# Kernel tuning notes

Hardware: AMD Instinct MI355X
Metric: run time of the kernel (lower is better)

Reference implementation:

```python
import jax, jax.numpy as jnp
import numpy as np

N_MEL, N_HID, N_ATT, N_TXT = 80, 1024, 640, 640

def lstm_cell(x, h, c, Wih, Whh, b):
    # torch LSTM gate order: i, f, g, o; b = b_ih + b_hh
    z = x @ Wih.T + h @ Whh.T + b
    i, f, g, o = jnp.split(z, 4, axis=-1)
    c = jax.nn.sigmoid(f) * c + jax.nn.sigmoid(i) * jnp.tanh(g)
    h = jax.nn.sigmoid(o) * jnp.tanh(c)
    return h, c

def setup_inputs() -> dict:
    key = jax.random.key(0)
    ks = jax.random.split(key, 32)
    s = 0.02
    p = {}
    p['residual'] = jax.random.normal(ks[0], (600, 1, N_MEL), jnp.float32)
    p['text'] = jax.random.normal(ks[1], (200, 1, N_TXT), jnp.float32)
    # attention LSTM (input n_mel -> hidden n_hid)
    p['Wih_a'] = jax.random.normal(ks[2], (4 * N_HID, N_MEL)) * s
    p['Whh_a'] = jax.random.normal(ks[3], (4 * N_HID, N_HID)) * s
    p['b_a'] = jax.random.normal(ks[4], (4 * N_HID,)) * s
    # attention projections (no bias)
    p['Wq'] = jax.random.normal(ks[5], (N_ATT, N_HID)) * s
    p['Wk'] = jax.random.normal(ks[6], (N_ATT, N_TXT)) * s
    p['Wv'] = jax.random.normal(ks[7], (N_ATT, N_TXT)) * s
    p['v_attn'] = jax.random.normal(ks[8], (N_ATT,)) * s
    # main 2-layer LSTM (input n_hid+n_att -> n_hid)
    p['Wih0'] = jax.random.normal(ks[9], (4 * N_HID, N_HID + N_ATT)) * s
    p['Whh0'] = jax.random.normal(ks[10], (4 * N_HID, N_HID)) * s
    p['b0'] = jax.random.normal(ks[11], (4 * N_HID,)) * s
    p['Wih1'] = jax.random.normal(ks[12], (4 * N_HID, N_HID)) * s
    p['Whh1'] = jax.random.normal(ks[13], (4 * N_HID, N_HID)) * s
    p['b1'] = jax.random.normal(ks[14], (4 * N_HID,)) * s
    # dense layer: two tanh linears
    p['Wd1'] = jax.random.normal(ks[15], (N_HID, N_HID)) * s
    p['bd1'] = jax.random.normal(ks[16], (N_HID,)) * s
    p['Wd2'] = jax.random.normal(ks[17], (N_HID, N_HID)) * s
    p['bd2'] = jax.random.normal(ks[18], (N_HID,)) * s
    # 1x1 conv == linear n_hid -> 2*n_mel
    p['Wc'] = jax.random.normal(ks[19], (2 * N_MEL, N_HID)) * s
    p['bc'] = jax.random.normal(ks[20], (2 * N_MEL,)) * s
    # gate layer
    p['Wg'] = jax.random.normal(ks[21], (1, N_HID + N_ATT)) * s
    p['bg'] = jax.random.normal(ks[22], (1,)) * s
    return p

def reference(residual, text, Wih_a, Whh_a, b_a, Wq, Wk, Wv, v_attn,
              Wih0, Whh0, b0, Wih1, Whh1, b1, Wd1, bd1, Wd2, bd2,
              Wc, bc, Wg, bg):
    T, B, n_mel = residual.shape
    H = Whh_a.shape[1]
    keys = text @ Wk.T          # (Tt, B, A)  precomputed, constant over steps
    vals = text @ Wv.T          # (Tt, B, A)
    res_flip = residual[::-1]   # AR_Back_Step flips time before the AR pass

    def step(carry, r_t):
        last_out, ha, ca, h0, c0, h1, c1 = carry
        ha, ca = lstm_cell(last_out, ha, ca, Wih_a, Whh_a, b_a)
        q = ha @ Wq.T                                   # (B, A)
        scores = jnp.tanh(q[None] + keys) @ v_attn      # (Tt, B)
        attn = jax.nn.softmax(scores, axis=0)
        ctx = jnp.einsum('tb,tba->ba', attn, vals)      # (B, A)
        dec_in = jnp.concatenate([ha, ctx], axis=-1)    # (B, H+A)
        h0, c0 = lstm_cell(dec_in, h0, c0, Wih0, Whh0, b0)
        h1, c1 = lstm_cell(h0, h1, c1, Wih1, Whh1, b1)
        d = jnp.tanh(jnp.tanh(h1 @ Wd1.T + bd1) @ Wd2.T + bd2)
        dec_out = d @ Wc.T + bc                         # (B, 2*n_mel)
        log_s, bb = dec_out[:, :n_mel], dec_out[:, n_mel:]
        out = (r_t - bb) * jnp.exp(-log_s)              # inverse affine coupling
        gate = jax.nn.sigmoid(dec_in @ Wg.T + bg)       # (B, 1)
        return (out, ha, ca, h0, c0, h1, c1), (out, gate)

    z = jnp.zeros((B, H), residual.dtype)
    init = (jnp.zeros((B, n_mel), residual.dtype), z, z, z, z, z, z)
    _, (outs, gates) = jax.lax.scan(step, init, res_flip)
    return outs[::-1], gates
```

## Files before the change

### kernel.cpp

```cpp
#include <hip/hip_runtime.h>
#include <hip/hip_bf16.h>
#include <math.h>

#define GBK 256
#define NT  512

constexpr int T_STEPS = 600;
constexpr int TXT     = 200;
constexpr int NMEL    = 80;
constexpr int H       = 1024;
constexpr int ATT     = 640;
constexpr int DIN     = H + ATT;
constexpr int GATE_B  = 200;
constexpr int NPH     = 8;
constexpr int NREP    = 8;

constexpr size_t O_WQ    = 0;
constexpr size_t O_WIHA  = O_WQ   + (size_t)ATT*H;
constexpr size_t O_WIH0  = O_WIHA + (size_t)4*H*NMEL;
constexpr size_t O_WHH1  = O_WIH0 + (size_t)4*H*DIN;
constexpr size_t O_WD1   = O_WHH1 + (size_t)4*H*H;
constexpr size_t O_WD2   = O_WD1  + (size_t)H*H;
constexpr size_t O_KEYS  = O_WD2  + (size_t)H*H;
constexpr size_t O_VALS  = O_KEYS + (size_t)TXT*ATT;
constexpr size_t O_END_U = O_VALS + (size_t)TXT*ATT;
constexpr size_t RBYTE   = ((O_END_U*2 + 255)/256)*256;
constexpr int RECN = NREP*NPH*GBK*8;

typedef unsigned short ushortT;
typedef ushortT us4 __attribute__((ext_vector_type(4)));
typedef ushortT us8 __attribute__((ext_vector_type(8)));
typedef unsigned uv2 __attribute__((ext_vector_type(2)));
typedef unsigned uv4 __attribute__((ext_vector_type(4)));

__device__ __forceinline__ float bf2f(ushortT u) {
  return __uint_as_float(((unsigned)u) << 16);
}
__device__ __forceinline__ ushortT f2bf(float x) {
  __hip_bfloat16 h = __float2bfloat16(x);
  ushortT u; __builtin_memcpy(&u, &h, 2); return u;
}
__device__ __forceinline__ us4 cvt4(float4 a) {
  return us4{ f2bf(a.x), f2bf(a.y), f2bf(a.z), f2bf(a.w) };
}
__device__ __forceinline__ float sigf(float x) { return 1.0f / (1.0f + expf(-x)); }
__device__ __forceinline__ float tanhfast(float x) {
  float e = __expf(2.0f * x);
  return (e - 1.0f) / (e + 1.0f);
}

__device__ __forceinline__ float red64(float v) {
  #pragma unroll
  for (int off = 32; off > 0; off >>= 1) v += __shfl_xor(v, off, 64);
  return v;
}

__device__ __forceinline__ unsigned* recptr(unsigned* R, int rep, int p, int b) {
  return R + ((size_t)((rep*NPH + p)*GBK + b) * 8);
}

__device__ __forceinline__ void rpub_pair(unsigned* R, int p, int b, int pairIdx,
                                          float v, unsigned e) {
  uv2 d; d.x = __float_as_uint(v); d.y = e;
  #pragma unroll
  for (int rep = 0; rep < NREP; ++rep) {
    unsigned* ptr = recptr(R, rep, p, b) + pairIdx*2;
    asm volatile("global_store_dwordx2 %0, %1, off sc0 sc1"
                 :: "v"(ptr), "v"(d) : "memory");
  }
}

template<int NCHK>
__device__ __forceinline__ float4 rwaitT(const unsigned* rec, unsigned e) {
  float4 o;
  if (NCHK == 1) {
    uv2 p;
    while (true) {
      asm volatile("global_load_dwordx2 %0, %1, off sc0 sc1\n\ts_waitcnt vmcnt(0)"
                   : "=v"(p) : "v"(rec) : "memory");
      if (p.y >= e) break;
      __builtin_amdgcn_s_sleep(1);
    }
    o.x = __uint_as_float(p.x); o.y = 0.f; o.z = 0.f; o.w = 0.f;
    return o;
  }
  uv4 lo, hi;
  const unsigned* r2 = rec + 4;
  while (true) {
    asm volatile("global_load_dwordx4 %0, %2, off sc0 sc1\n\t"
                 "global_load_dwordx4 %1, %3, off sc0 sc1\n\t"
                 "s_waitcnt vmcnt(0)"
                 : "=&v"(lo), "=&v"(hi) : "v"(rec), "v"(r2) : "memory");
    bool ok = (lo.y >= e) && (lo.w >= e);
    if (NCHK >= 3) ok = ok && (hi.y >= e);
    if (NCHK >= 4) ok = ok && (hi.w >= e);
    if (ok) break;
    __builtin_amdgcn_s_sleep(1);
  }
  o.x = __uint_as_float(lo.x); o.y = __uint_as_float(lo.z);
  o.z = __uint_as_float(hi.x); o.w = __uint_as_float(hi.z);
  return o;
}

__device__ __forceinline__ float dotbf(const ushortT* __restrict__ Wrow,
                                       const float* __restrict__ v, int lane) {
  const us4* w4 = (const us4*)Wrow;
  const float4* v4 = (const float4*)v;
  float s = 0.f;
  #pragma unroll
  for (int c = 0; c < 4; ++c) {
    us4 w = w4[c*64 + lane];
    float4 x = v4[c*64 + lane];
    s += bf2f(w[0])*x.x + bf2f(w[1])*x.y + bf2f(w[2])*x.z + bf2f(w[3])*x.w;
  }
  return s;
}
__device__ __forceinline__ float dotf(const float* __restrict__ Wrow,
                                      const float* __restrict__ v, int lane) {
  const float4* w4 = (const float4*)Wrow;
  const float4* v4 = (const float4*)v;
  float s = 0.f;
  #pragma unroll
  for (int c = 0; c < 4; ++c) {
    float4 w = w4[c*64 + lane], x = v4[c*64 + lane];
    s += w.x*x.x + w.y*x.y + w.z*x.z + w.w*x.w;
  }
  return s;
}
__device__ __forceinline__ float dot200(const float* __restrict__ a,
                                        const float* __restrict__ e, int lane) {
  float s = a[lane]*e[lane] + a[64+lane]*e[64+lane] + a[128+lane]*e[128+lane];
  if (lane < 8) s += a[192+lane]*e[192+lane];
  return s;
}

__global__ void conv_bf16(const float* __restrict__ src, ushortT* __restrict__ dst, size_t n) {
  size_t i  = blockIdx.x * (size_t)blockDim.x + threadIdx.x;
  size_t st = (size_t)gridDim.x * blockDim.x;
  for (; i < n; i += st) dst[i] = f2bf(src[i]);
}

__global__ void prep_kv(const float* __restrict__ text, const float* __restrict__ Wk,
                        const float* __restrict__ Wv, ushortT* __restrict__ keys,
                        ushortT* __restrict__ vals) {
  __shared__ float tx[ATT];
  const int t = blockIdx.x;
  for (int i = threadIdx.x; i < ATT; i += blockDim.x) tx[i] = text[(size_t)t*ATT + i];
  __syncthreads();
  for (int a = threadIdx.x; a < 2*ATT; a += blockDim.x) {
    const int which = (a >= ATT);
    const int ar = a - which*ATT;
    const float4* w4 = (const float4*)((which ? Wv : Wk) + (size_t)ar*ATT);
    const float4* t4 = (const float4*)tx;
    float s = 0.f;
    for (int i = 0; i < ATT/4; ++i) {
      float4 w = w4[i], x = t4[i];
      s += w.x*x.x + w.y*x.y + w.z*x.z + w.w*x.w;
    }
    (which ? vals : keys)[(size_t)t*ATT + ar] = f2bf(s);
  }
}

__global__ void prep_zero(unsigned* R) {
  int i = blockIdx.x * blockDim.x + threadIdx.x;
  if (i < RECN) R[i] = 0u;
}

__global__ void __launch_bounds__(NT, 1)
ar_persist(const float* __restrict__ residual,
           const float* __restrict__ Whh_a, const float* __restrict__ Whh0g,
           const float* __restrict__ Wih1g,
           const float* __restrict__ b_a, const float* __restrict__ v_attn,
           const float* __restrict__ b0, const float* __restrict__ b1,
           const float* __restrict__ bd1, const float* __restrict__ bd2,
           const float* __restrict__ Wc, const float* __restrict__ bc,
           const float* __restrict__ Wg, const float* __restrict__ bg,
           float* __restrict__ out, void* __restrict__ wsraw)
{
  const int tid  = threadIdx.x;
  const int bid  = blockIdx.x;
  const int wid  = tid >> 6;
  const int lane = tid & 63;
  const int rep  = bid & (NREP - 1);

  const ushortT* uws = (const ushortT*)wsraw;
  unsigned* R = (unsigned*)((char*)wsraw + RBYTE);

  const ushortT* wq    = uws + O_WQ;
  const ushortT* wiha  = uws + O_WIHA;
  const ushortT* wih0s = uws + O_WIH0;
  const ushortT* whh1s = uws + O_WHH1;
  const ushortT* wd1   = uws + O_WD1;
  const ushortT* wd2   = uws + O_WD2;
  const ushortT* keys  = uws + O_KEYS;
  const ushortT* vals  = uws + O_VALS;

  const int ub = bid*4;
  const int rlA = wid*2, rlB = wid*2 + 1;
  const int zrA = (rlA>>2)*H + ub + (rlA&3);
  const int zrB = (rlB>>2)*H + ub + (rlB&3);

  __shared__ __align__(16) ushortT lWhha[16*H];
  __shared__ __align__(16) ushortT lWhh0[16*H];
  __shared__ __align__(16) ushortT lWih1[16*H];
  __shared__ __align__(16) ushortT lWd1[4*H];
  __shared__ __align__(16) ushortT lWd2[4*H];
  __shared__ __align__(16) ushortT lWq[3*H];
  __shared__ __align__(16) float   V0[16*TXT];
  __shared__ __align__(16) float   vg[TXT];
  __shared__ __align__(16) float   lvatt[ATT];
  __shared__ __align__(16) float   lha[H], lh0[H], lh1[H];
  __shared__ __align__(16) float   shq[ATT];
  __shared__ __align__(16) float   shv[H];
  __shared__ __align__(16) float   shx[128];
  __shared__ __align__(16) float   sce[TXT + 64];
  __shared__ float zl[16], zp[16], zaH[16], z0H[16], z1H[16];
  __shared__ float cA[4], c0S[4], c1S[4], misc2[4];

  {
    us4* dA = (us4*)lWhha; us4* dC = (us4*)lWhh0; us4* dD = (us4*)lWih1;
    #pragma unroll
    for (int j = 0; j < 2; ++j) {
      const int rl = wid*2 + j;
      const int zr = (rl>>2)*H + ub + (rl&3);
      #pragma unroll
      for (int c = 0; c < 4; ++c) {
        const int ei = c*64 + lane;
        dA[rl*256 + ei] = cvt4(*(const float4*)(Whh_a + (size_t)zr*H + ei*4));
        dC[rl*256 + ei] = cvt4(*(const float4*)(Whh0g + (size_t)zr*H + ei*4));
        dD[rl*256 + ei] = cvt4(*(const float4*)(Wih1g + (size_t)zr*H + ei*4));
      }
    }
    if (wid < 4) {
      const us4* s1 = (const us4*)(wd1 + (size_t)(bid*4 + wid)*H);
      #pragma unroll
      for (int c = 0; c < 4; ++c)
        ((us4*)lWd1)[wid*256 + c*64 + lane] = s1[c*64 + lane];
    } else {
      const int w = wid - 4;
      const us4* s2 = (const us4*)(wd2 + (size_t)(bid*4 + w)*H);
      #pragma unroll
      for (int c = 0; c < 4; ++c)
        ((us4*)lWd2)[w*256 + c*64 + lane] = s2[c*64 + lane];
    }
    for (int w = 0; w < 3; ++w) {
      const int qr = bid + w*GBK;
      if (qr < ATT) {
        const us4* sq = (const us4*)(wq + (size_t)qr*H);
        for (int i = tid; i < 256; i += NT) ((us4*)lWq)[w*256 + i] = sq[i];
      }
    }
    for (int i = tid; i < ATT; i += NT) lvatt[i] = v_attn[i];
  }
  for (int idx = tid; idx < 16*TXT; idx += NT) {
    const int r = idx / TXT, t = idx - r*TXT;
    const int zr = (r>>2)*H + ub + (r&3);
    const us8* wp = (const us8*)(wih0s + (size_t)zr*DIN + H);
    const us8* vp = (const us8*)(vals + (size_t)t*ATT);
    float acc = 0.f;
    for (int c = 0; c < ATT/8; ++c) {
      us8 w = wp[c], v = vp[c];
      #pragma unroll
      for (int e2 = 0; e2 < 8; ++e2) acc += bf2f(w[e2]) * bf2f(v[e2]);
    }
    V0[r*TXT + t] = acc;
  }
  if (bid == GATE_B) {
    for (int t = tid; t < TXT; t += NT) {
      const float4* wp = (const float4*)(Wg + H);
      const us4* vp = (const us4*)(vals + (size_t)t*ATT);
      float acc = 0.f;
      for (int c = 0; c < ATT/4; ++c) {
        float4 w = wp[c]; us4 v = vp[c];
        acc += w.x*bf2f(v[0]) + w.y*bf2f(v[1]) + w.z*bf2f(v[2]) + w.w*bf2f(v[3]);
      }
      vg[t] = acc;
    }
  }
  if (tid < 16) { zaH[tid] = 0.f; z0H[tid] = 0.f; z1H[tid] = 0.f; }
  if (tid < 4)  { cA[tid] = 0.f; c0S[tid] = 0.f; c1S[tid] = 0.f; }
  __syncthreads();

  for (int s = 0; s < T_STEPS; ++s) {
    const unsigned e = (unsigned)s + 1u;

    if (tid < NMEL) {
      float4 r = rwaitT<1>(recptr(R, rep, 0, tid), (unsigned)s);
      shx[tid] = r.x;
    }
    __syncthreads();
    {
      float sA = 0.f, sB = 0.f;
      if (lane < 20) {
        float4 xv = ((const float4*)shx)[lane];
        us4 w = ((const us4*)wiha)[(size_t)zrA*20 + lane];
        sA = bf2f(w[0])*xv.x + bf2f(w[1])*xv.y + bf2f(w[2])*xv.z + bf2f(w[3])*xv.w;
        w = ((const us4*)wiha)[(size_t)zrB*20 + lane];
        sB = bf2f(w[0])*xv.x + bf2f(w[1])*xv.y + bf2f(w[2])*xv.z + bf2f(w[3])*xv.w;
      }
      sA = red64(sA) + zaH[rlA] + b_a[zrA];
      sB = red64(sB) + zaH[rlB] + b_a[zrB];
      if (lane == 0) { zl[rlA] = sA; zl[rlB] = sB; }
    }
    __syncthreads();
    if (tid < 4) {
      float c = sigf(zl[4+tid])*cA[tid] + sigf(zl[tid])*tanhf(zl[8+tid]);
      cA[tid] = c;
      rpub_pair(R, 1, bid, tid, sigf(zl[12+tid])*tanhf(c), e);
    }

    if (tid < GBK) {
      float4 r = rwaitT<4>(recptr(R, rep, 1, tid), e);
      ((float4*)lha)[tid] = r;
    }
    __syncthreads();
    if (wid < 3) {
      if (wid < 2 || bid < ATT - 2*GBK) {
        float sq = red64(dotbf(lWq + wid*H, lha, lane));
        if (lane == 0) rpub_pair(R, 2, bid, wid, sq, e);
      }
    }
    if (bid == GATE_B && wid == 3) {
      float sg = red64(dotf(Wg, lha, lane));
      if (lane == 0) misc2[0] = sg;
    }
    {
      const bool earlyzp = (wid >= 4) || (bid >= TXT);
      if (earlyzp) {
        float sA = red64(dotbf(wih0s + (size_t)zrA*DIN, lha, lane)) + z0H[rlA] + b0[zrA];
        float sB = red64(dotbf(wih0s + (size_t)zrB*DIN, lha, lane)) + z0H[rlB] + b0[zrB];
        if (lane == 0) { zp[rlA] = sA; zp[rlB] = sB; }
      }
      if (bid < TXT) {
        if (tid < GBK) {
          float4 r = (tid < 128) ? rwaitT<3>(recptr(R, rep, 2, tid), e)
                                 : rwaitT<2>(recptr(R, rep, 2, tid), e);
          shq[tid] = r.x; shq[256 + tid] = r.y;
          if (tid < 128) shq[512 + tid] = r.z;
        }
        __syncthreads();
        if (wid == 0) {
          const us4* kp = (const us4*)(keys + (size_t)bid*ATT);
          float ss = 0.f;
          for (int c = lane; c < 160; c += 64) {
            us4 k = kp[c];
            float4 q4 = ((const float4*)shq)[c];
            float4 v4 = ((const float4*)lvatt)[c];
            ss += tanhfast(bf2f(k[0]) + q4.x)*v4.x + tanhfast(bf2f(k[1]) + q4.y)*v4.y
                + tanhfast(bf2f(k[2]) + q4.z)*v4.z + tanhfast(bf2f(k[3]) + q4.w)*v4.w;
          }
          ss = red64(ss);
          if (lane == 0) rpub_pair(R, 3, bid, 0, ss, e);
        }
      }
      if (!earlyzp) {
        float sA = red64(dotbf(wih0s + (size_t)zrA*DIN, lha, lane)) + z0H[rlA] + b0[zrA];
        float sB = red64(dotbf(wih0s + (size_t)zrB*DIN, lha, lane)) + z0H[rlB] + b0[zrB];
        if (lane == 0) { zp[rlA] = sA; zp[rlB] = sB; }
      }
    }

    if (tid < TXT) {
      float4 r = rwaitT<1>(recptr(R, rep, 3, tid), e);
      sce[tid] = __expf(r.x);
    }
    __syncthreads();
    if (wid == 0) {
      float pz = sce[lane] + sce[64+lane] + sce[128+lane]
               + (lane < 8 ? sce[192+lane] : 0.f);
      pz = red64(pz);
      if (lane == 0) misc2[1] = 1.0f / pz;
    }
    {
      float rA = red64(dot200(V0 + rlA*TXT, sce, lane));
      float rB = red64(dot200(V0 + rlB*TXT, sce, lane));
      if (lane == 0) { zl[rlA] = rA; zl[rlB] = rB; }
    }
    __syncthreads();
    if (tid < 4) {
      const float invZ = misc2[1];
      float iv = zl[tid]*invZ    + zp[tid];
      float fv = zl[4+tid]*invZ  + zp[4+tid];
      float gv = zl[8+tid]*invZ  + zp[8+tid];
      float ov = zl[12+tid]*invZ + zp[12+tid];
      float c = sigf(fv)*c0S[tid] + sigf(iv)*tanhf(gv);
      c0S[tid] = c;
      rpub_pair(R, 4, bid, tid, sigf(ov)*tanhf(c), e);
    }
    if (bid == GATE_B && wid == 3) {
      float sg = red64(dot200(vg, sce, lane)) * misc2[1];
      if (lane == 0) out[T_STEPS*NMEL + s] = sigf(sg + misc2[0] + bg[0]);
    }

    if (tid < GBK) {
      float4 r = rwaitT<4>(recptr(R, rep, 4, tid), e);
      ((float4*)lh0)[tid] = r;
    }
    __syncthreads();
    {
      float sA = red64(dotbf(lWih1 + rlA*H, lh0, lane)) + z1H[rlA] + b1[zrA];
      float sB = red64(dotbf(lWih1 + rlB*H, lh0, lane)) + z1H[rlB] + b1[zrB];
      if (lane == 0) { zl[rlA] = sA; zl[rlB] = sB; }
    }
    __syncthreads();
    if (tid < 4) {
      float c = sigf(zl[4+tid])*c1S[tid] + sigf(zl[tid])*tanhf(zl[8+tid]);
      c1S[tid] = c;
      rpub_pair(R, 5, bid, tid, sigf(zl[12+tid])*tanhf(c), e);
    }
    {
      float pA = red64(dotbf(lWhh0 + rlA*H, lh0, lane));
      float pB = red64(dotbf(lWhh0 + rlB*H, lh0, lane));
      if (lane == 0) { z0H[rlA] = pA; z0H[rlB] = pB; }
    }

    if (tid < GBK) {
      float4 r = rwaitT<4>(recptr(R, rep, 5, tid), e);
      ((float4*)lh1)[tid] = r;
    }
    __syncthreads();
    if (wid < 4) {
      const int r = bid*4 + wid;
      float t6 = red64(dotbf(lWd1 + wid*H, lh1, lane)) + bd1[r];
      if (lane == 0) rpub_pair(R, 6, bid, wid, tanhf(t6), e);
    }
    {
      float pA = red64(dotbf(lWhha + rlA*H, lha, lane));
      float pB = red64(dotbf(lWhha + rlB*H, lha, lane));
      if (lane == 0) { zaH[rlA] = pA; zaH[rlB] = pB; }
    }

    if (tid < GBK) {
      float4 r = rwaitT<4>(recptr(R, rep, 6, tid), e);
      ((float4*)shv)[tid] = r;
    }
    __syncthreads();
    if (wid < 4) {
      const int r = bid*4 + wid;
      float t7 = red64(dotbf(lWd2 + wid*H, shv, lane)) + bd2[r];
      if (lane == 0) rpub_pair(R, 7, bid, wid, tanhf(t7), e);
    }
    {
      float pA = red64(dotbf(whh1s + (size_t)zrA*H, lh1, lane));
      float pB = red64(dotbf(whh1s + (size_t)zrB*H, lh1, lane));
      if (lane == 0) { z1H[rlA] = pA; z1H[rlB] = pB; }
    }

    if (bid < NMEL) {
      __syncthreads();
      if (tid < GBK) {
        float4 r = rwaitT<4>(recptr(R, rep, 7, tid), e);
        ((float4*)shv)[tid] = r;
      }
      __syncthreads();
      if (wid < 2) {
        const int r = wid*NMEL + bid;
        float s8 = red64(dotf(Wc + (size_t)r*H, shv, lane)) + bc[r];
        if (lane == 0) misc2[2 + wid] = s8;
      }
      __syncthreads();
      if (tid == 0) {
        const int idx = T_STEPS - 1 - s;
        const float r = residual[idx*NMEL + bid];
        const float o = (r - misc2[3]) * expf(-misc2[2]);
        out[idx*NMEL + bid] = o;
        rpub_pair(R, 0, bid, 0, o, e);
      }
    }
  }
}

extern "C" void kernel_launch(void* const* d_in, const int* in_sizes, int n_in,
                              void* d_out, int out_size, void* d_ws, size_t ws_size,
                              hipStream_t stream) {
  const float* residual = (const float*)d_in[0];
  const float* text   = (const float*)d_in[1];
  const float* Wih_a  = (const float*)d_in[2];
  const float* Whh_a  = (const float*)d_in[3];
  const float* b_a    = (const float*)d_in[4];
  const float* Wq     = (const float*)d_in[5];
  const float* Wk     = (const float*)d_in[6];
  const float* Wv     = (const float*)d_in[7];
  const float* v_attn = (const float*)d_in[8];
  const float* Wih0   = (const float*)d_in[9];
  const float* Whh0   = (const float*)d_in[10];
  const float* b0     = (const float*)d_in[11];
  const float* Wih1   = (const float*)d_in[12];
  const float* Whh1   = (const float*)d_in[13];
  const float* b1     = (const float*)d_in[14];
  const float* Wd1    = (const float*)d_in[15];
  const float* bd1    = (const float*)d_in[16];
  const float* Wd2    = (const float*)d_in[17];
  const float* bd2    = (const float*)d_in[18];
  const float* Wc     = (const float*)d_in[19];
  const float* bc     = (const float*)d_in[20];
  const float* Wg     = (const float*)d_in[21];
  const float* bg     = (const float*)d_in[22];
  float* out = (float*)d_out;

  char* wsb = (char*)d_ws;
  ushortT*  u = (ushortT*)wsb;
  unsigned* R = (unsigned*)(wsb + RBYTE);

  conv_bf16<<<1024, 256, 0, stream>>>(Wq,    u + O_WQ,   (size_t)ATT*H);
  conv_bf16<<<1024, 256, 0, stream>>>(Wih_a, u + O_WIHA, (size_t)4*H*NMEL);
  conv_bf16<<<1024, 256, 0, stream>>>(Wih0,  u + O_WIH0, (size_t)4*H*DIN);
  conv_bf16<<<1024, 256, 0, stream>>>(Whh1,  u + O_WHH1, (size_t)4*H*H);
  conv_bf16<<<1024, 256, 0, stream>>>(Wd1,   u + O_WD1,  (size_t)H*H);
  conv_bf16<<<1024, 256, 0, stream>>>(Wd2,   u + O_WD2,  (size_t)H*H);
  prep_kv<<<TXT, 256, 0, stream>>>(text, Wk, Wv, u + O_KEYS, u + O_VALS);
  prep_zero<<<(RECN + 255)/256, 256, 0, stream>>>(R);

  ar_persist<<<GBK, NT, 0, stream>>>(residual, Whh_a, Whh0, Wih1,
      b_a, v_attn, b0, b1, bd1, bd2, Wc, bc, Wg, bg, out, d_ws);
}
```

Baseline: 11.26 ms.

## Pack LSTM hidden states as bf16 and poll from two replicas per block

After: 14.62 ms. 29.8% more time.

```diff
diff --git a/kernel.cpp b/kernel.cpp
--- a/kernel.cpp
+++ b/kernel.cpp
@@ -69,7 +69,31 @@
                  :: "v"(ptr), "v"(d) : "memory");
   }
 }
-
+__device__ __forceinline__ void rpub_h(unsigned* R, int p, int b,
+                                       unsigned h01, unsigned h23, unsigned e) {
+  uv4 d; d.x = h01; d.y = e; d.z = h23; d.w = e;
+  #pragma unroll
+  for (int rep = 0; rep < NREP; ++rep) {
+    unsigned* ptr = recptr(R, rep, p, b);
+    asm volatile("global_store_dwordx4 %0, %1, off sc0 sc1"
+                 :: "v"(ptr), "v"(d) : "memory");
+  }
+}
+__device__ __forceinline__ float4 rwait_h(const unsigned* rec, unsigned e) {
+  uv4 r;
+  while (true) {
+    asm volatile("global_load_dwordx4 %0, %1, off sc0 sc1\n\ts_waitcnt vmcnt(0)"
+                 : "=v"(r) : "v"(rec) : "memory");
+    if (r.y >= e && r.w >= e) break;
+    __builtin_amdgcn_s_sleep(1);
+  }
+  float4 o;
+  o.x = bf2f((ushortT)(r.x & 0xffffu));
+  o.y = bf2f((ushortT)(r.x >> 16));
+  o.z = bf2f((ushortT)(r.z & 0xffffu));
+  o.w = bf2f((ushortT)(r.z >> 16));
+  return o;
+}
 template<int NCHK>
 __device__ __forceinline__ float4 rwaitT(const unsigned* rec, unsigned e) {
   float4 o;
@@ -182,6 +206,7 @@
   const int wid  = tid >> 6;
   const int lane = tid & 63;
   const int rep  = bid & (NREP - 1);
+  const int rep2 = (bid + 4) & (NREP - 1);
 
   const ushortT* uws = (const ushortT*)wsraw;
   unsigned* R = (unsigned*)((char*)wsraw + RBYTE);
@@ -284,9 +309,13 @@
   for (int s = 0; s < T_STEPS; ++s) {
     const unsigned e = (unsigned)s + 1u;
 
-    if (tid < NMEL) {
-      float4 r = rwaitT<1>(recptr(R, rep, 0, tid), (unsigned)s);
-      shx[tid] = r.x;
+    {
+      const int t = tid & 255;
+      if (t < NMEL) {
+        if (tid >= 256) __builtin_amdgcn_s_sleep(4);
+        float4 r = rwaitT<1>(recptr(R, (tid >= 256) ? rep2 : rep, 0, t), (unsigned)s);
+        shx[t] = r.x;
+      }
     }
     __syncthreads();
     {
@@ -306,12 +335,17 @@
     if (tid < 4) {
       float c = sigf(zl[4+tid])*cA[tid] + sigf(zl[tid])*tanhf(zl[8+tid]);
       cA[tid] = c;
-      rpub_pair(R, 1, bid, tid, sigf(zl[12+tid])*tanhf(c), e);
-    }
-
-    if (tid < GBK) {
-      float4 r = rwaitT<4>(recptr(R, rep, 1, tid), e);
-      ((float4*)lha)[tid] = r;
+      unsigned hb = (unsigned)f2bf(sigf(zl[12+tid])*tanhf(c));
+      unsigned p01 = __shfl(hb, 0, 64) | (__shfl(hb, 1, 64) << 16);
+      unsigned p23 = __shfl(hb, 2, 64) | (__shfl(hb, 3, 64) << 16);
+      if (tid == 0) rpub_h(R, 1, bid, p01, p23, e);
+    }
+
+    {
+      const int t = tid & 255;
+      if (tid >= 256) __builtin_amdgcn_s_sleep(4);
+      float4 r = rwait_h(recptr(R, (tid >= 256) ? rep2 : rep, 1, t), e);
+      ((float4*)lha)[t] = r;
     }
     __syncthreads();
     if (wid < 3) {
@@ -332,11 +366,14 @@
         if (lane == 0) { zp[rlA] = sA; zp[rlB] = sB; }
       }
       if (bid < TXT) {
-        if (tid < GBK) {
-          float4 r = (tid < 128) ? rwaitT<3>(recptr(R, rep, 2, tid), e)
-                                 : rwaitT<2>(recptr(R, rep, 2, tid), e);
-          shq[tid] = r.x; shq[256 + tid] = r.y;
-          if (tid < 128) shq[512 + tid] = r.z;
+        {
+          const int t = tid & 255;
+          if (tid >= 256) __builtin_amdgcn_s_sleep(4);
+          const int rp = (tid >= 256) ? rep2 : rep;
+          float4 r = (t < 128) ? rwaitT<3>(recptr(R, rp, 2, t), e)
+                               : rwaitT<2>(recptr(R, rp, 2, t), e);
+          shq[t] = r.x; shq[256 + t] = r.y;
+          if (t < 128) shq[512 + t] = r.z;
         }
         __syncthreads();
         if (wid == 0) {
@@ -360,41 +397,46 @@
       }
     }
 
-    if (tid < TXT) {
-      float4 r = rwaitT<1>(recptr(R, rep, 3, tid), e);
-      sce[tid] = __expf(r.x);
-    }
-    __syncthreads();
-    if (wid == 0) {
+    {
+      const int t = tid & 255;
+      if (t < TXT) {
+        if (tid >= 256) __builtin_amdgcn_s_sleep(4);
+        float4 r = rwaitT<1>(recptr(R, (tid >= 256) ? rep2 : rep, 3, t), e);
+        sce[t] = __expf(r.x);
+      }
+    }
+    __syncthreads();
+    float invZ;
+    {
       float pz = sce[lane] + sce[64+lane] + sce[128+lane]
                + (lane < 8 ? sce[192+lane] : 0.f);
       pz = red64(pz);
-      if (lane == 0) misc2[1] = 1.0f / pz;
+      invZ = 1.0f / pz;
     }
     {
       float rA = red64(dot200(V0 + rlA*TXT, sce, lane));
       float rB = red64(dot200(V0 + rlB*TXT, sce, lane));
-      if (lane == 0) { zl[rlA] = rA; zl[rlB] = rB; }
+      if (lane == 0) { zl[rlA] = rA*invZ + zp[rlA]; zl[rlB] = rB*invZ + zp[rlB]; }
     }
     __syncthreads();
     if (tid < 4) {
-      const float invZ = misc2[1];
-      float iv = zl[tid]*invZ    + zp[tid];
-      float fv = zl[4+tid]*invZ  + zp[4+tid];
-      float gv = zl[8+tid]*invZ  + zp[8+tid];
-      float ov = zl[12+tid]*invZ + zp[12+tid];
-      float c = sigf(fv)*c0S[tid] + sigf(iv)*tanhf(gv);
+      float c = sigf(zl[4+tid])*c0S[tid] + sigf(zl[tid])*tanhf(zl[8+tid]);
       c0S[tid] = c;
-      rpub_pair(R, 4, bid, tid, sigf(ov)*tanhf(c), e);
+      unsigned hb = (unsigned)f2bf(sigf(zl[12+tid])*tanhf(c));
+      unsigned p01 = __shfl(hb, 0, 64) | (__shfl(hb, 1, 64) << 16);
+      unsigned p23 = __shfl(hb, 2, 64) | (__shfl(hb, 3, 64) << 16);
+      if (tid == 0) rpub_h(R, 4, bid, p01, p23, e);
     }
     if (bid == GATE_B && wid == 3) {
-      float sg = red64(dot200(vg, sce, lane)) * misc2[1];
+      float sg = red64(dot200(vg, sce, lane)) * invZ;
       if (lane == 0) out[T_STEPS*NMEL + s] = sigf(sg + misc2[0] + bg[0]);
     }
 
-    if (tid < GBK) {
-      float4 r = rwaitT<4>(recptr(R, rep, 4, tid), e);
-      ((float4*)lh0)[tid] = r;
+    {
+      const int t = tid & 255;
+      if (tid >= 256) __builtin_amdgcn_s_sleep(4);
+      float4 r = rwait_h(recptr(R, (tid >= 256) ? rep2 : rep, 4, t), e);
+      ((float4*)lh0)[t] = r;
     }
     __syncthreads();
     {
@@ -406,7 +448,10 @@
     if (tid < 4) {
       float c = sigf(zl[4+tid])*c1S[tid] + sigf(zl[tid])*tanhf(zl[8+tid]);
       c1S[tid] = c;
-      rpub_pair(R, 5, bid, tid, sigf(zl[12+tid])*tanhf(c), e);
+      unsigned hb = (unsigned)f2bf(sigf(zl[12+tid])*tanhf(c));
+      unsigned p01 = __shfl(hb, 0, 64) | (__shfl(hb, 1, 64) << 16);
+      unsigned p23 = __shfl(hb, 2, 64) | (__shfl(hb, 3, 64) << 16);
+      if (tid == 0) rpub_h(R, 5, bid, p01, p23, e);
     }
     {
       float pA = red64(dotbf(lWhh0 + rlA*H, lh0, lane));
@@ -414,9 +459,11 @@
       if (lane == 0) { z0H[rlA] = pA; z0H[rlB] = pB; }
     }
 
-    if (tid < GBK) {
-      float4 r = rwaitT<4>(recptr(R, rep, 5, tid), e);
-      ((float4*)lh1)[tid] = r;
+    {
+      const int t = tid & 255;
+      if (tid >= 256) __builtin_amdgcn_s_sleep(4);
+      float4 r = rwait_h(recptr(R, (tid >= 256) ? rep2 : rep, 5, t), e);
+      ((float4*)lh1)[t] = r;
     }
     __syncthreads();
     if (wid < 4) {
@@ -430,9 +477,11 @@
       if (lane == 0) { zaH[rlA] = pA; zaH[rlB] = pB; }
     }
 
-    if (tid < GBK) {
-      float4 r = rwaitT<4>(recptr(R, rep, 6, tid), e);
-      ((float4*)shv)[tid] = r;
+    {
+      const int t = tid & 255;
+      if (tid >= 256) __builtin_amdgcn_s_sleep(4);
+      float4 r = rwaitT<4>(recptr(R, (tid >= 256) ? rep2 : rep, 6, t), e);
+      ((float4*)shv)[t] = r;
     }
     __syncthreads();
     if (wid < 4) {
@@ -448,23 +497,23 @@
 
     if (bid < NMEL) {
       __syncthreads();
-      if (tid < GBK) {
-        float4 r = rwaitT<4>(recptr(R, rep, 7, tid), e);
-        ((float4*)shv)[tid] = r;
+      {
+        const int t = tid & 255;
+        if (tid >= 256) __builtin_amdgcn_s_sleep(4);
+        float4 r = rwaitT<4>(recptr(R, (tid >= 256) ? rep2 : rep, 7, t), e);
+        ((float4*)shv)[t] = r;
       }
       __syncthreads();
-      if (wid < 2) {
-        const int r = wid*NMEL + bid;
-        float s8 = red64(dotf(Wc + (size_t)r*H, shv, lane)) + bc[r];
-        if (lane == 0) misc2[2 + wid] = s8;
-      }
-      __syncthreads();
-      if (tid == 0) {
-        const int idx = T_STEPS - 1 - s;
-        const float r = residual[idx*NMEL + bid];
-        const float o = (r - misc2[3]) * expf(-misc2[2]);
-        out[idx*NMEL + bid] = o;
-        rpub_pair(R, 0, bid, 0, o, e);
+      if (wid == 0) {
+        float sl = red64(dotf(Wc + (size_t)bid*H, shv, lane)) + bc[bid];
+        float sb = red64(dotf(Wc + (size_t)(NMEL + bid)*H, shv, lane)) + bc[NMEL + bid];
+        if (lane == 0) {
+          const int idx = T_STEPS - 1 - s;
+          const float r = residual[idx*NMEL + bid];
+          const float o = (r - sb) * expf(-sl);
+          out[idx*NMEL + bid] = o;
+          rpub_pair(R, 0, bid, 0, o, e);
+        }
       }
     }
   }
```
